# Performance work log

Hardware: AMD Instinct MI355X
Metric: run time of the kernel (lower is better)

The kernel has to match this reference:

```python
import jax, jax.numpy as jnp
import numpy as np

PAD = 20  # (41 - 1) // 2, matches ReflectionPad2d(20)
CHANNELS = 6


def _matlab_gauss2d(shape=(41, 41), sigma=10.0):
    m, n = [(s - 1.0) / 2.0 for s in shape]
    y, x = np.ogrid[-m:m + 1, -n:n + 1]
    h = np.exp(-(x * x + y * y) / (2.0 * sigma * sigma))
    h[h < np.finfo(h.dtype).eps * h.max()] = 0
    s = h.sum()
    if s != 0:
        h /= s
    return h


def setup_inputs() -> dict:
    key = jax.random.key(0)
    x = jax.random.normal(key, (16, CHANNELS, 512, 512), dtype=jnp.float32)
    k = _matlab_gauss2d((41, 41), 10.0)  # [41, 41]
    # depthwise weight [C, 1, 41, 41], same kernel repeated per channel
    weight = jnp.asarray(np.repeat(k[None, None], CHANNELS, axis=0), dtype=jnp.float32)
    return {"x": x, "weight": weight}


def reference(x, weight):
    # reflect-pad H and W by 20 (PyTorch ReflectionPad2d semantics == jnp 'reflect')
    xp = jnp.pad(x, ((0, 0), (0, 0), (PAD, PAD), (PAD, PAD)), mode="reflect")
    # depthwise conv: feature_group_count = C, weight is [C, 1, kH, kW]
    out = jax.lax.conv_general_dilated(
        xp, weight,
        window_strides=(1, 1),
        padding="VALID",
        dimension_numbers=("NCHW", "OIHW", "NCHW"),
        feature_group_count=CHANNELS,
    )
    return out  # [B, C, H, W]
```

## Files before the change

### kernel.cpp

```cpp
#include <hip/hip_runtime.h>

#define KS 41
#define PAD 20
#define H 512
#define W 512
#define CH 6

__device__ __forceinline__ int reflect_idx(int i, int n) {
    if (i < 0) i = -i;
    if (i >= n) i = 2 * n - 2 - i;
    return i;
}

__device__ __forceinline__ int reflect511(int i) {
    return (H - 1) - abs((H - 1) - abs(i));
}

__device__ __forceinline__ float uniform_f(float v) {
    return __uint_as_float(__builtin_amdgcn_readfirstlane(__float_as_uint(v)));
}

__device__ __forceinline__ void load_coeffs(const float* __restrict__ w, int c,
                                            int lane, float gk[KS]) {
    float my = 0.f;
    if (lane < KS) {
        const float* wr = w + (size_t)c * KS * KS + (size_t)lane * KS;
        #pragma unroll
        for (int j = 0; j < KS; ++j) my += wr[j];
    }
    #pragma unroll
    for (int j = 0; j < KS; ++j)
        gk[j] = __uint_as_float(__builtin_amdgcn_readlane(__float_as_uint(my), j));
}

__device__ __forceinline__ void st4_swz(float* L, int q, float4 v) {
    const int pq = q ^ ((q >> 3) & 7);
    *(float4*)(L + 4 * pq) = v;
}
__device__ __forceinline__ float4 ld4_swz(const float* L, int q) {
    const int pq = q ^ ((q >> 3) & 7);
    return *(const float4*)(L + 4 * pq);
}
__device__ __forceinline__ int swz(int p) {
    return p ^ (((p >> 5) & 7) << 2);
}

__global__ __launch_bounds__(256, 4)
void gauss_h_kernel(const float* __restrict__ x, const float* __restrict__ w,
                    float* __restrict__ ws) {
    __shared__ float rowbuf[4][560];

    const int tid = threadIdx.x;
    const int wv  = tid >> 6;
    const int l   = tid & 63;
    const int img = blockIdx.y;
    const int c   = img % CH;
    const int row = blockIdx.x * 4 + wv;

    float gk[KS];
    load_coeffs(w, c, l, gk);

    const float4* src4 = (const float4*)(x + ((size_t)img * H + row) * W);
    float4 v0 = src4[l];
    float4 v1 = src4[l + 64];
    float* L = rowbuf[wv];
    st4_swz(L, l + 5, v0);
    st4_swz(L, l + 69, v1);
    __builtin_amdgcn_wave_barrier();

    if (l < 2 * PAD) {
        const int dstp = (l < PAD) ? l        : (512 + l);
        const int srcp = (l < PAD) ? (40 - l) : (550 - l);
        float hv = L[swz(srcp)];
        L[swz(dstp)] = hv;
    }
    __builtin_amdgcn_wave_barrier();

    float win[48];
    #pragma unroll
    for (int m = 0; m < 12; ++m) {
        float4 q = ld4_swz(L, 2 * l + m);
        win[4 * m + 0] = q.x; win[4 * m + 1] = q.y;
        win[4 * m + 2] = q.z; win[4 * m + 3] = q.w;
    }

    float acc[8];
    #pragma unroll
    for (int i = 0; i < 8; ++i) acc[i] = 0.f;
    #pragma unroll
    for (int j = 0; j < KS; ++j) {
        const float gj = gk[j];
        #pragma unroll
        for (int i = 0; i < 8; ++i) acc[i] += gj * win[j + i];
    }

    float* dst = ws + ((size_t)img * H + row) * W + 8 * l;
    *(float4*)(dst)     = make_float4(acc[0], acc[1], acc[2], acc[3]);
    *(float4*)(dst + 4) = make_float4(acc[4], acc[5], acc[6], acc[7]);
}

#define VTW 64
#define VTH 128
#define VTMPH (VTH + 2 * PAD)

__global__ __launch_bounds__(256, 3)
void gauss_v_kernel(const float* __restrict__ ws, const float* __restrict__ w,
                    float* __restrict__ out) {
    __shared__ float tmp[VTMPH * VTW];

    const int tid = threadIdx.x;
    const int bx  = blockIdx.x;
    const int by  = blockIdx.y;
    const int img = blockIdx.z;
    const int c   = img % CH;

    float gk[KS];
    load_coeffs(w, c, tid & 63, gk);

    const float* sbase = ws + (size_t)img * H * W + bx * VTW;
    for (int idx = tid; idx < VTMPH * 16; idx += 256) {
        const int r  = idx >> 4;
        const int q  = idx & 15;
        const int sr = reflect511(by * VTH - PAD + r);
        float4 v = *(const float4*)(sbase + (size_t)sr * W + 4 * q);
        *(float4*)&tmp[r * VTW + 4 * q] = v;
    }
    __syncthreads();

    const int lx = tid & 63;
    const int yg = tid >> 6;
    float* o = out + ((size_t)img * H + by * VTH) * W + bx * VTW + lx;

    #pragma unroll
    for (int cc = 0; cc < 2; ++cc) {
        const int yc = yg * 32 + cc * 16;
        float col[56];
        #pragma unroll
        for (int i = 0; i < 56; ++i)
            col[i] = tmp[(yc + i) * VTW + lx];
        #pragma unroll
        for (int y = 0; y < 16; ++y) {
            float s = 0.f;
            #pragma unroll
            for (int j = 0; j < KS; ++j) s += gk[j] * col[y + j];
            o[(size_t)(yc + y) * W] = s;
        }
    }
}

#define TW 64
#define TH 128
#define TMPH (TH + 2 * PAD)

__global__ __launch_bounds__(256, 3)
void gauss_blur_fused_kernel(const float* __restrict__ x,
                             const float* __restrict__ w,
                             float* __restrict__ out) {
    __shared__ float g_s[KS];
    __shared__ float tmp[TMPH * TW];

    const int tid = threadIdx.x;
    const int bx = blockIdx.x, by = blockIdx.y, bz = blockIdx.z;
    const int c = bz % CH;

    if (tid < KS) {
        const float* wr = w + (size_t)c * KS * KS + (size_t)tid * KS;
        float s = 0.f;
        #pragma unroll
        for (int j = 0; j < KS; ++j) s += wr[j];
        g_s[tid] = s;
    }
    __syncthreads();

    float gr[KS];
    #pragma unroll
    for (int j = 0; j < KS; ++j) gr[j] = uniform_f(g_s[j]);

    const size_t img_off = (size_t)bz * (H * W);
    const float* img = x + img_off;
    const int x_tile = bx * TW;

    for (int gid = tid; gid < TMPH * (TW / 8); gid += 256) {
        const int r  = gid >> 3;
        const int gx = gid & 7;
        const int gy = reflect_idx(by * TH - PAD + r, H);
        const int x0 = x_tile + gx * 8;
        const float* row = img + (size_t)gy * W;

        float buf[48];
        if (x0 >= PAD && x0 + 27 <= W - 1) {
            const float4* p = (const float4*)(row + x0 - PAD);
            #pragma unroll
            for (int m = 0; m < 12; ++m) {
                float4 v = p[m];
                buf[4 * m + 0] = v.x; buf[4 * m + 1] = v.y;
                buf[4 * m + 2] = v.z; buf[4 * m + 3] = v.w;
            }
        } else {
            #pragma unroll
            for (int j = 0; j < 48; ++j)
                buf[j] = row[reflect_idx(x0 - PAD + j, W)];
        }

        float s[8];
        #pragma unroll
        for (int k = 0; k < 8; ++k) s[k] = 0.f;
        #pragma unroll
        for (int j = 0; j < KS; ++j) {
            #pragma unroll
            for (int k = 0; k < 8; ++k) s[k] += gr[j] * buf[j + k];
        }
        float* dstp = &tmp[r * TW + gx * 8];
        #pragma unroll
        for (int k = 0; k < 8; ++k) dstp[k] = s[k];
    }
    __syncthreads();

    const int lx = tid & 63;
    const int yg = tid >> 6;
    float* o = out + img_off;

    #pragma unroll
    for (int cc = 0; cc < 2; ++cc) {
        const int yc = yg * 32 + cc * 16;
        float col[56];
        #pragma unroll
        for (int i = 0; i < 56; ++i)
            col[i] = tmp[(yc + i) * TW + lx];
        #pragma unroll
        for (int y = 0; y < 16; ++y) {
            float s = 0.f;
            #pragma unroll
            for (int j = 0; j < KS; ++j) s += gr[j] * col[y + j];
            o[(size_t)(by * TH + yc + y) * W + x_tile + lx] = s;
        }
    }
}

extern "C" void kernel_launch(void* const* d_in, const int* in_sizes, int n_in,
                              void* d_out, int out_size, void* d_ws, size_t ws_size,
                              hipStream_t stream) {
    const float* x = (const float*)d_in[0];
    const float* w = (const float*)d_in[1];
    float* out = (float*)d_out;
    (void)in_sizes; (void)n_in; (void)out_size;

    const size_t need = (size_t)16 * CH * H * W * sizeof(float);
    if (ws_size >= need) {
        float* ws = (float*)d_ws;
        gauss_h_kernel<<<dim3(H / 4, 16 * CH), 256, 0, stream>>>(x, w, ws);
        gauss_v_kernel<<<dim3(W / VTW, H / VTH, 16 * CH), 256, 0, stream>>>(ws, w, out);
    } else {
        dim3 grid(W / TW, H / TH, 16 * CH);
        gauss_blur_fused_kernel<<<grid, 256, 0, stream>>>(x, w, out);
    }
}
```

Measured before the change: 243.6 us.

## Fuse horizontal and vertical blur passes via shared-memory ring buffer

Replaces the two-kernel separable blur, which wrote and reread a full-size global workspace, with one kernel per 128x256 tile. Each tile computes horizontal-pass rows into a circular shared-memory ring and consumes them in 32-row chunks for the vertical pass. The vertical pass uses 4x4 register blocking on float4 reads. This removes the intermediate global traffic but recomputes halo rows per tile, uses a small grid with per-chunk block barriers, and drops the fallback path.

```diff
diff --git a/kernel.cpp b/kernel.cpp
--- a/kernel.cpp
+++ b/kernel.cpp
@@ -6,18 +6,15 @@
 #define W 512
 #define CH 6
 
-__device__ __forceinline__ int reflect_idx(int i, int n) {
-    if (i < 0) i = -i;
-    if (i >= n) i = 2 * n - 2 - i;
-    return i;
-}
+#define WS   128
+#define HS   256
+#define RB   32
+#define NIT  (HS / RB)
+#define RING 72
+#define RSTR 132
 
 __device__ __forceinline__ int reflect511(int i) {
     return (H - 1) - abs((H - 1) - abs(i));
-}
-
-__device__ __forceinline__ float uniform_f(float v) {
-    return __uint_as_float(__builtin_amdgcn_readfirstlane(__float_as_uint(v)));
 }
 
 __device__ __forceinline__ void load_coeffs(const float* __restrict__ w, int c,
@@ -33,55 +30,26 @@
         gk[j] = __uint_as_float(__builtin_amdgcn_readlane(__float_as_uint(my), j));
 }
 
-__device__ __forceinline__ void st4_swz(float* L, int q, float4 v) {
-    const int pq = q ^ ((q >> 3) & 7);
-    *(float4*)(L + 4 * pq) = v;
-}
-__device__ __forceinline__ float4 ld4_swz(const float* L, int q) {
-    const int pq = q ^ ((q >> 3) & 7);
-    return *(const float4*)(L + 4 * pq);
-}
-__device__ __forceinline__ int swz(int p) {
-    return p ^ (((p >> 5) & 7) << 2);
-}
-
-__global__ __launch_bounds__(256, 4)
-void gauss_h_kernel(const float* __restrict__ x, const float* __restrict__ w,
-                    float* __restrict__ ws) {
-    __shared__ float rowbuf[4][560];
-
-    const int tid = threadIdx.x;
-    const int wv  = tid >> 6;
-    const int l   = tid & 63;
-    const int img = blockIdx.y;
-    const int c   = img % CH;
-    const int row = blockIdx.x * 4 + wv;
-
-    float gk[KS];
-    load_coeffs(w, c, l, gk);
-
-    const float4* src4 = (const float4*)(x + ((size_t)img * H + row) * W);
-    float4 v0 = src4[l];
-    float4 v1 = src4[l + 64];
-    float* L = rowbuf[wv];
-    st4_swz(L, l + 5, v0);
-    st4_swz(L, l + 69, v1);
-    __builtin_amdgcn_wave_barrier();
-
-    if (l < 2 * PAD) {
-        const int dstp = (l < PAD) ? l        : (512 + l);
-        const int srcp = (l < PAD) ? (40 - l) : (550 - l);
-        float hv = L[swz(srcp)];
-        L[swz(dstp)] = hv;
-    }
-    __builtin_amdgcn_wave_barrier();
+__device__ __forceinline__ void htask(const float* __restrict__ img,
+                                      float* __restrict__ ring,
+                                      const float gk[KS],
+                                      int id, int s, int Y0, int x0) {
+    const int ry = reflect511(Y0 - PAD + id);
+    const float* row = img + (size_t)ry * W;
+    const int xs = x0 + 8 * s - PAD;
 
     float win[48];
-    #pragma unroll
-    for (int m = 0; m < 12; ++m) {
-        float4 q = ld4_swz(L, 2 * l + m);
-        win[4 * m + 0] = q.x; win[4 * m + 1] = q.y;
-        win[4 * m + 2] = q.z; win[4 * m + 3] = q.w;
+    if (xs >= 0 && xs <= W - 48) {
+        const float4* p = (const float4*)(row + xs);
+        #pragma unroll
+        for (int m = 0; m < 12; ++m) {
+            float4 v = p[m];
+            win[4 * m + 0] = v.x; win[4 * m + 1] = v.y;
+            win[4 * m + 2] = v.z; win[4 * m + 3] = v.w;
+        }
+    } else {
+        #pragma unroll
+        for (int j = 0; j < 48; ++j) win[j] = row[reflect511(xs + j)];
     }
 
     float acc[8];
@@ -89,151 +57,85 @@
     for (int i = 0; i < 8; ++i) acc[i] = 0.f;
     #pragma unroll
     for (int j = 0; j < KS; ++j) {
-        const float gj = gk[j];
+        const float g = gk[j];
         #pragma unroll
-        for (int i = 0; i < 8; ++i) acc[i] += gj * win[j + i];
+        for (int i = 0; i < 8; ++i) acc[i] += g * win[j + i];
     }
 
-    float* dst = ws + ((size_t)img * H + row) * W + 8 * l;
-    *(float4*)(dst)     = make_float4(acc[0], acc[1], acc[2], acc[3]);
-    *(float4*)(dst + 4) = make_float4(acc[4], acc[5], acc[6], acc[7]);
+    const int slot = id % RING;
+    float* d = ring + slot * RSTR + 8 * s;
+    *(float4*)(d)     = make_float4(acc[0], acc[1], acc[2], acc[3]);
+    *(float4*)(d + 4) = make_float4(acc[4], acc[5], acc[6], acc[7]);
 }
 
-#define VTW 64
-#define VTH 128
-#define VTMPH (VTH + 2 * PAD)
-
-__global__ __launch_bounds__(256, 3)
-void gauss_v_kernel(const float* __restrict__ ws, const float* __restrict__ w,
-                    float* __restrict__ out) {
-    __shared__ float tmp[VTMPH * VTW];
+__global__ __launch_bounds__(256, 4)
+void gauss_fused_kernel(const float* __restrict__ x, const float* __restrict__ w,
+                        float* __restrict__ out) {
+    __shared__ float ring[RING * RSTR];
 
     const int tid = threadIdx.x;
     const int bx  = blockIdx.x;
     const int by  = blockIdx.y;
     const int img = blockIdx.z;
     const int c   = img % CH;
+    const int x0  = bx * WS;
+    const int Y0  = by * HS;
 
     float gk[KS];
     load_coeffs(w, c, tid & 63, gk);
 
-    const float* sbase = ws + (size_t)img * H * W + bx * VTW;
-    for (int idx = tid; idx < VTMPH * 16; idx += 256) {
-        const int r  = idx >> 4;
-        const int q  = idx & 15;
-        const int sr = reflect511(by * VTH - PAD + r);
-        float4 v = *(const float4*)(sbase + (size_t)sr * W + 4 * q);
-        *(float4*)&tmp[r * VTW + 4 * q] = v;
-    }
-    __syncthreads();
+    const float* imgp = x + (size_t)img * H * W;
 
-    const int lx = tid & 63;
-    const int yg = tid >> 6;
-    float* o = out + ((size_t)img * H + by * VTH) * W + bx * VTW + lx;
+    for (int t = tid; t < 2 * PAD * 16; t += 256)
+        htask(imgp, ring, gk, t >> 4, t & 15, Y0, x0);
 
-    #pragma unroll
-    for (int cc = 0; cc < 2; ++cc) {
-        const int yc = yg * 32 + cc * 16;
-        float col[56];
-        #pragma unroll
-        for (int i = 0; i < 56; ++i)
-            col[i] = tmp[(yc + i) * VTW + lx];
-        #pragma unroll
-        for (int y = 0; y < 16; ++y) {
-            float s = 0.f;
+    const int cg = tid & 31;
+    const int rg = tid >> 5;
+    float* obase = out + ((size_t)img * H + (size_t)(Y0 + 4 * rg)) * W + x0 + 4 * cg;
+
+    for (int k = 0; k < NIT; ++k) {
+        {
+            const int base = 2 * PAD + RB * k;
+            htask(imgp, ring, gk, base + (tid >> 4), tid & 15, Y0, x0);
+            const int t2 = tid + 256;
+            htask(imgp, ring, gk, base + (t2 >> 4), t2 & 15, Y0, x0);
+        }
+        __syncthreads();
+
+        {
+            float acc[4][4];
             #pragma unroll
-            for (int j = 0; j < KS; ++j) s += gk[j] * col[y + j];
-            o[(size_t)(yc + y) * W] = s;
+            for (int i = 0; i < 4; ++i)
+                #pragma unroll
+                for (int jj = 0; jj < 4; ++jj) acc[i][jj] = 0.f;
+
+            const int s0 = (RB * k + 4 * rg) % RING;
+            int fo = s0 * RSTR + 4 * cg;
+            #pragma unroll
+            for (int j = 0; j < 44; ++j) {
+                const float4 v = *(const float4*)(ring + fo);
+                fo += RSTR;
+                if (fo >= RING * RSTR) fo -= RING * RSTR;
+                #pragma unroll
+                for (int rr = 0; rr < 4; ++rr) {
+                    const int tap = j - rr;
+                    if (tap >= 0 && tap < KS) {
+                        const float g = gk[tap];
+                        acc[rr][0] += g * v.x;
+                        acc[rr][1] += g * v.y;
+                        acc[rr][2] += g * v.z;
+                        acc[rr][3] += g * v.w;
+                    }
+                }
+            }
+
+            float* o = obase + (size_t)(RB * k) * W;
+            #pragma unroll
+            for (int rr = 0; rr < 4; ++rr)
+                *(float4*)(o + (size_t)rr * W) =
+                    make_float4(acc[rr][0], acc[rr][1], acc[rr][2], acc[rr][3]);
         }
-    }
-}
-
-#define TW 64
-#define TH 128
-#define TMPH (TH + 2 * PAD)
-
-__global__ __launch_bounds__(256, 3)
-void gauss_blur_fused_kernel(const float* __restrict__ x,
-                             const float* __restrict__ w,
-                             float* __restrict__ out) {
-    __shared__ float g_s[KS];
-    __shared__ float tmp[TMPH * TW];
-
-    const int tid = threadIdx.x;
-    const int bx = blockIdx.x, by = blockIdx.y, bz = blockIdx.z;
-    const int c = bz % CH;
-
-    if (tid < KS) {
-        const float* wr = w + (size_t)c * KS * KS + (size_t)tid * KS;
-        float s = 0.f;
-        #pragma unroll
-        for (int j = 0; j < KS; ++j) s += wr[j];
-        g_s[tid] = s;
-    }
-    __syncthreads();
-
-    float gr[KS];
-    #pragma unroll
-    for (int j = 0; j < KS; ++j) gr[j] = uniform_f(g_s[j]);
-
-    const size_t img_off = (size_t)bz * (H * W);
-    const float* img = x + img_off;
-    const int x_tile = bx * TW;
-
-    for (int gid = tid; gid < TMPH * (TW / 8); gid += 256) {
-        const int r  = gid >> 3;
-        const int gx = gid & 7;
-        const int gy = reflect_idx(by * TH - PAD + r, H);
-        const int x0 = x_tile + gx * 8;
-        const float* row = img + (size_t)gy * W;
-
-        float buf[48];
-        if (x0 >= PAD && x0 + 27 <= W - 1) {
-            const float4* p = (const float4*)(row + x0 - PAD);
-            #pragma unroll
-            for (int m = 0; m < 12; ++m) {
-                float4 v = p[m];
-                buf[4 * m + 0] = v.x; buf[4 * m + 1] = v.y;
-                buf[4 * m + 2] = v.z; buf[4 * m + 3] = v.w;
-            }
-        } else {
-            #pragma unroll
-            for (int j = 0; j < 48; ++j)
-                buf[j] = row[reflect_idx(x0 - PAD + j, W)];
-        }
-
-        float s[8];
-        #pragma unroll
-        for (int k = 0; k < 8; ++k) s[k] = 0.f;
-        #pragma unroll
-        for (int j = 0; j < KS; ++j) {
-            #pragma unroll
-            for (int k = 0; k < 8; ++k) s[k] += gr[j] * buf[j + k];
-        }
-        float* dstp = &tmp[r * TW + gx * 8];
-        #pragma unroll
-        for (int k = 0; k < 8; ++k) dstp[k] = s[k];
-    }
-    __syncthreads();
-
-    const int lx = tid & 63;
-    const int yg = tid >> 6;
-    float* o = out + img_off;
-
-    #pragma unroll
-    for (int cc = 0; cc < 2; ++cc) {
-        const int yc = yg * 32 + cc * 16;
-        float col[56];
-        #pragma unroll
-        for (int i = 0; i < 56; ++i)
-            col[i] = tmp[(yc + i) * TW + lx];
-        #pragma unroll
-        for (int y = 0; y < 16; ++y) {
-            float s = 0.f;
-            #pragma unroll
-            for (int j = 0; j < KS; ++j) s += gr[j] * col[y + j];
-            o[(size_t)(by * TH + yc + y) * W + x_tile + lx] = s;
-        }
+        __syncthreads();
     }
 }
 
@@ -243,15 +145,7 @@
     const float* x = (const float*)d_in[0];
     const float* w = (const float*)d_in[1];
     float* out = (float*)d_out;
-    (void)in_sizes; (void)n_in; (void)out_size;
+    (void)in_sizes; (void)n_in; (void)out_size; (void)d_ws; (void)ws_size;
 
-    const size_t need = (size_t)16 * CH * H * W * sizeof(float);
-    if (ws_size >= need) {
-        float* ws = (float*)d_ws;
-        gauss_h_kernel<<<dim3(H / 4, 16 * CH), 256, 0, stream>>>(x, w, ws);
-        gauss_v_kernel<<<dim3(W / VTW, H / VTH, 16 * CH), 256, 0, stream>>>(ws, w, out);
-    } else {
-        dim3 grid(W / TW, H / TH, 16 * CH);
-        gauss_blur_fused_kernel<<<grid, 256, 0, stream>>>(x, w, out);
-    }
+    gauss_fused_kernel<<<dim3(W / WS, H / HS, 16 * CH), 256, 0, stream>>>(x, w, out);
 }
```

After: 811.1 us. +232.9%, slower.

## Replace LDS staging with direct global-load register sliding windows in both passes

Applied to the files above, without the earlier changes.

The horizontal pass drops its per-wave LDS row buffer. Each lane now reads its 44-element window straight from global memory as float4 and computes 4 outputs per 256-wide half, looping over 4 rows per wave. The vertical pass drops its LDS tile. Each thread streams 56 reflected rows of one float4 column and accumulates 16 output rows in registers, with occupancy lowered to 2 via launch bounds. The fused fallback kernel is also rewritten to accumulate taps as data arrives rather than buffering 48 values. This trades LDS traffic and barriers for redundant overlapping global/L2 reads and higher register pressure.

```diff
diff --git a/kernel.cpp b/kernel.cpp
--- a/kernel.cpp
+++ b/kernel.cpp
@@ -6,14 +6,14 @@
 #define W 512
 #define CH 6
 
+__device__ __forceinline__ int reflect511(int i) {
+    return (H - 1) - abs((H - 1) - abs(i));
+}
+
 __device__ __forceinline__ int reflect_idx(int i, int n) {
     if (i < 0) i = -i;
     if (i >= n) i = 2 * n - 2 - i;
     return i;
-}
-
-__device__ __forceinline__ int reflect511(int i) {
-    return (H - 1) - abs((H - 1) - abs(i));
 }
 
 __device__ __forceinline__ float uniform_f(float v) {
@@ -33,119 +33,106 @@
         gk[j] = __uint_as_float(__builtin_amdgcn_readlane(__float_as_uint(my), j));
 }
 
-__device__ __forceinline__ void st4_swz(float* L, int q, float4 v) {
-    const int pq = q ^ ((q >> 3) & 7);
-    *(float4*)(L + 4 * pq) = v;
-}
-__device__ __forceinline__ float4 ld4_swz(const float* L, int q) {
-    const int pq = q ^ ((q >> 3) & 7);
-    return *(const float4*)(L + 4 * pq);
-}
-__device__ __forceinline__ int swz(int p) {
-    return p ^ (((p >> 5) & 7) << 2);
-}
+#define HROWS 16
 
 __global__ __launch_bounds__(256, 4)
 void gauss_h_kernel(const float* __restrict__ x, const float* __restrict__ w,
                     float* __restrict__ ws) {
-    __shared__ float rowbuf[4][560];
-
     const int tid = threadIdx.x;
+    const int l   = tid & 63;
     const int wv  = tid >> 6;
-    const int l   = tid & 63;
     const int img = blockIdx.y;
     const int c   = img % CH;
-    const int row = blockIdx.x * 4 + wv;
+    const int R0  = blockIdx.x * HROWS + wv * 4;
 
     float gk[KS];
     load_coeffs(w, c, l, gk);
 
-    const float4* src4 = (const float4*)(x + ((size_t)img * H + row) * W);
-    float4 v0 = src4[l];
-    float4 v1 = src4[l + 64];
-    float* L = rowbuf[wv];
-    st4_swz(L, l + 5, v0);
-    st4_swz(L, l + 69, v1);
-    __builtin_amdgcn_wave_barrier();
-
-    if (l < 2 * PAD) {
-        const int dstp = (l < PAD) ? l        : (512 + l);
-        const int srcp = (l < PAD) ? (40 - l) : (550 - l);
-        float hv = L[swz(srcp)];
-        L[swz(dstp)] = hv;
-    }
-    __builtin_amdgcn_wave_barrier();
-
-    float win[48];
-    #pragma unroll
-    for (int m = 0; m < 12; ++m) {
-        float4 q = ld4_swz(L, 2 * l + m);
-        win[4 * m + 0] = q.x; win[4 * m + 1] = q.y;
-        win[4 * m + 2] = q.z; win[4 * m + 3] = q.w;
-    }
-
-    float acc[8];
-    #pragma unroll
-    for (int i = 0; i < 8; ++i) acc[i] = 0.f;
-    #pragma unroll
-    for (int j = 0; j < KS; ++j) {
-        const float gj = gk[j];
-        #pragma unroll
-        for (int i = 0; i < 8; ++i) acc[i] += gj * win[j + i];
-    }
-
-    float* dst = ws + ((size_t)img * H + row) * W + 8 * l;
-    *(float4*)(dst)     = make_float4(acc[0], acc[1], acc[2], acc[3]);
-    *(float4*)(dst + 4) = make_float4(acc[4], acc[5], acc[6], acc[7]);
-}
-
-#define VTW 64
-#define VTH 128
-#define VTMPH (VTH + 2 * PAD)
-
-__global__ __launch_bounds__(256, 3)
+    const float* imgp = x + (size_t)img * H * W;
+    float* wsp = ws + (size_t)img * H * W;
+
+    for (int rr = 0; rr < 4; ++rr) {
+        const int row = R0 + rr;
+        const float* rp = imgp + (size_t)row * W;
+        float* op = wsp + (size_t)row * W;
+
+        #pragma unroll
+        for (int hh = 0; hh < 2; ++hh) {
+            const int x0 = 256 * hh + 4 * l;
+            const int xs = x0 - PAD;
+            float a0 = 0.f, a1 = 0.f, a2 = 0.f, a3 = 0.f;
+
+            if (xs >= 0 && xs <= W - 44) {
+                const float4* p = (const float4*)(rp + xs);
+                #pragma unroll
+                for (int m = 0; m < 11; ++m) {
+                    const float4 q = p[m];
+                    const float f[4] = {q.x, q.y, q.z, q.w};
+                    #pragma unroll
+                    for (int t = 0; t < 4; ++t) {
+                        const int k = 4 * m + t;
+                        if (k <= 40)            a0 += gk[k]     * f[t];
+                        if (k >= 1 && k <= 41)  a1 += gk[k - 1] * f[t];
+                        if (k >= 2 && k <= 42)  a2 += gk[k - 2] * f[t];
+                        if (k >= 3)             a3 += gk[k - 3] * f[t];
+                    }
+                }
+            } else {
+                #pragma unroll
+                for (int k = 0; k < 44; ++k) {
+                    const float f = rp[reflect511(xs + k)];
+                    if (k <= 40)            a0 += gk[k]     * f;
+                    if (k >= 1 && k <= 41)  a1 += gk[k - 1] * f;
+                    if (k >= 2 && k <= 42)  a2 += gk[k - 2] * f;
+                    if (k >= 3)             a3 += gk[k - 3] * f;
+                }
+            }
+            *(float4*)(op + x0) = make_float4(a0, a1, a2, a3);
+        }
+    }
+}
+
+#define VROWS 16
+
+__global__ __launch_bounds__(256, 2)
 void gauss_v_kernel(const float* __restrict__ ws, const float* __restrict__ w,
                     float* __restrict__ out) {
-    __shared__ float tmp[VTMPH * VTW];
-
     const int tid = threadIdx.x;
-    const int bx  = blockIdx.x;
-    const int by  = blockIdx.y;
-    const int img = blockIdx.z;
+    const int img = blockIdx.y;
     const int c   = img % CH;
+    const int t   = blockIdx.x * 256 + tid;
+    const int cq  = t & 127;
+    const int rg  = t >> 7;
+    const int y0  = rg * VROWS;
 
     float gk[KS];
     load_coeffs(w, c, tid & 63, gk);
 
-    const float* sbase = ws + (size_t)img * H * W + bx * VTW;
-    for (int idx = tid; idx < VTMPH * 16; idx += 256) {
-        const int r  = idx >> 4;
-        const int q  = idx & 15;
-        const int sr = reflect511(by * VTH - PAD + r);
-        float4 v = *(const float4*)(sbase + (size_t)sr * W + 4 * q);
-        *(float4*)&tmp[r * VTW + 4 * q] = v;
-    }
-    __syncthreads();
-
-    const int lx = tid & 63;
-    const int yg = tid >> 6;
-    float* o = out + ((size_t)img * H + by * VTH) * W + bx * VTW + lx;
-
-    #pragma unroll
-    for (int cc = 0; cc < 2; ++cc) {
-        const int yc = yg * 32 + cc * 16;
-        float col[56];
-        #pragma unroll
-        for (int i = 0; i < 56; ++i)
-            col[i] = tmp[(yc + i) * VTW + lx];
-        #pragma unroll
-        for (int y = 0; y < 16; ++y) {
-            float s = 0.f;
-            #pragma unroll
-            for (int j = 0; j < KS; ++j) s += gk[j] * col[y + j];
-            o[(size_t)(yc + y) * W] = s;
-        }
-    }
+    const float* wsp = ws + (size_t)img * H * W + 4 * cq;
+    float* op = out + (size_t)img * H * W + 4 * cq;
+
+    float4 acc[VROWS];
+    #pragma unroll
+    for (int i = 0; i < VROWS; ++i) acc[i] = make_float4(0.f, 0.f, 0.f, 0.f);
+
+    #pragma unroll
+    for (int i = 0; i < VROWS + 2 * PAD; ++i) {
+        const int r = reflect511(y0 - PAD + i);
+        const float4 v = *(const float4*)(wsp + (size_t)r * W);
+        #pragma unroll
+        for (int oi = 0; oi < VROWS; ++oi) {
+            const int j = i - oi;
+            if (j >= 0 && j < KS) {
+                const float g = gk[j];
+                acc[oi].x += g * v.x; acc[oi].y += g * v.y;
+                acc[oi].z += g * v.z; acc[oi].w += g * v.w;
+            }
+        }
+    }
+
+    #pragma unroll
+    for (int oi = 0; oi < VROWS; ++oi)
+        *(float4*)(op + (size_t)(y0 + oi) * W) = acc[oi];
 }
 
 #define TW 64
@@ -187,28 +174,36 @@
         const int x0 = x_tile + gx * 8;
         const float* row = img + (size_t)gy * W;
 
-        float buf[48];
+        float s[8];
+        #pragma unroll
+        for (int k = 0; k < 8; ++k) s[k] = 0.f;
+
         if (x0 >= PAD && x0 + 27 <= W - 1) {
             const float4* p = (const float4*)(row + x0 - PAD);
             #pragma unroll
             for (int m = 0; m < 12; ++m) {
-                float4 v = p[m];
-                buf[4 * m + 0] = v.x; buf[4 * m + 1] = v.y;
-                buf[4 * m + 2] = v.z; buf[4 * m + 3] = v.w;
+                const float4 v = p[m];
+                const float f[4] = {v.x, v.y, v.z, v.w};
+                #pragma unroll
+                for (int t = 0; t < 4; ++t) {
+                    const int pos = 4 * m + t;
+                    #pragma unroll
+                    for (int k = 0; k < 8; ++k) {
+                        const int tap = pos - k;
+                        if (tap >= 0 && tap < KS) s[k] += gr[tap] * f[t];
+                    }
+                }
             }
         } else {
             #pragma unroll
-            for (int j = 0; j < 48; ++j)
-                buf[j] = row[reflect_idx(x0 - PAD + j, W)];
-        }
-
-        float s[8];
-        #pragma unroll
-        for (int k = 0; k < 8; ++k) s[k] = 0.f;
-        #pragma unroll
-        for (int j = 0; j < KS; ++j) {
-            #pragma unroll
-            for (int k = 0; k < 8; ++k) s[k] += gr[j] * buf[j + k];
+            for (int pos = 0; pos < 48; ++pos) {
+                const float f = row[reflect_idx(x0 - PAD + pos, W)];
+                #pragma unroll
+                for (int k = 0; k < 8; ++k) {
+                    const int tap = pos - k;
+                    if (tap >= 0 && tap < KS) s[k] += gr[tap] * f;
+                }
+            }
         }
         float* dstp = &tmp[r * TW + gx * 8];
         #pragma unroll
@@ -248,8 +243,8 @@
     const size_t need = (size_t)16 * CH * H * W * sizeof(float);
     if (ws_size >= need) {
         float* ws = (float*)d_ws;
-        gauss_h_kernel<<<dim3(H / 4, 16 * CH), 256, 0, stream>>>(x, w, ws);
-        gauss_v_kernel<<<dim3(W / VTW, H / VTH, 16 * CH), 256, 0, stream>>>(ws, w, out);
+        gauss_h_kernel<<<dim3(H / HROWS, 16 * CH), 256, 0, stream>>>(x, w, ws);
+        gauss_v_kernel<<<dim3(16, 16 * CH), 256, 0, stream>>>(ws, w, out);
     } else {
         dim3 grid(W / TW, H / TH, 16 * CH);
         gauss_blur_fused_kernel<<<grid, 256, 0, stream>>>(x, w, out);
```

After: 451.6 us. 1.85x slower.
